# Kernel optimization log

Measured on AMD Instinct MI355X. Metric: run time of the kernel, lower is better.

The kernel has to match this reference:

```python
import jax, jax.numpy as jnp
import numpy as np

B, S, D, H = 2, 2048, 768, 12
HD = D // H
WINDOW = 64  # local_attention // 2
ROPE_THETA = 10000.0
NEG = -1e9


def setup_inputs() -> dict:
    key = jax.random.key(0)
    k1, k2, k3 = jax.random.split(key, 3)
    hidden_states = jax.random.normal(k1, (B, S, D), dtype=jnp.float32)
    Wqkv_w = jax.random.normal(k2, (3 * D, D), dtype=jnp.float32) * (D ** -0.5)
    Wo_w = jax.random.normal(k3, (D, D), dtype=jnp.float32) * (D ** -0.5)
    position_ids = jnp.broadcast_to(jnp.arange(S, dtype=jnp.int64 if jax.config.jax_enable_x64 else jnp.int32), (B, S))
    # additive sliding-window mask: 0 inside window, -1e9 outside (matches torch ModernBert mask construction)
    idx = np.arange(S)
    dist = np.abs(idx[:, None] - idx[None, :])
    sliding_window_mask = jnp.asarray(np.where(dist <= WINDOW, 0.0, NEG), dtype=jnp.float32)[None, None]  # [1,1,S,S]
    return {"hidden_states": hidden_states, "Wqkv_w": Wqkv_w, "Wo_w": Wo_w,
            "sliding_window_mask": sliding_window_mask, "position_ids": position_ids}


def _rotate_half(x):
    x1, x2 = jnp.split(x, 2, axis=-1)
    return jnp.concatenate([-x2, x1], axis=-1)


def reference(hidden_states, Wqkv_w, Wo_w, sliding_window_mask, position_ids):
    b, s, d = hidden_states.shape
    qkv = hidden_states @ Wqkv_w.T                      # [B,S,3D]
    qkv = qkv.reshape(b, s, 3, H, HD)
    q = qkv[:, :, 0].transpose(0, 2, 1, 3)              # [B,H,S,HD]
    k = qkv[:, :, 1].transpose(0, 2, 1, 3)
    v = qkv[:, :, 2].transpose(0, 2, 1, 3)
    # RoPE
    inv_freq = 1.0 / (ROPE_THETA ** (jnp.arange(0, HD, 2, dtype=jnp.float32) / HD))  # [HD/2]
    freqs = position_ids.astype(jnp.float32)[..., None] * inv_freq                   # [B,S,HD/2]
    emb = jnp.concatenate([freqs, freqs], axis=-1)                                   # [B,S,HD]
    cos = jnp.cos(emb)[:, None]                          # [B,1,S,HD]
    sin = jnp.sin(emb)[:, None]
    q = q * cos + _rotate_half(q) * sin
    k = k * cos + _rotate_half(k) * sin
    scale = HD ** -0.5
    scores = jnp.einsum('bhqd,bhkd->bhqk', q, k) * scale + sliding_window_mask       # [B,H,S,S]
    attn = jax.nn.softmax(scores.astype(jnp.float32), axis=-1).astype(q.dtype)
    out = jnp.einsum('bhqk,bhkd->bhqd', attn, v)         # [B,H,S,HD]
    out = out.transpose(0, 2, 1, 3).reshape(b, s, d)     # [B,S,D]
    return out @ Wo_w.T
```

## Files before the change

kernel.cpp:

```cpp
#include <hip/hip_runtime.h>
#include <hip/hip_bf16.h>
#include <cmath>

#define B_   2
#define S_   2048
#define D_   768
#define H_   12
#define HD_  64
#define WIN_ 64

typedef __bf16 bf16x8 __attribute__((ext_vector_type(8)));
typedef __bf16 bf16x4 __attribute__((ext_vector_type(4)));
typedef float  f32x4  __attribute__((ext_vector_type(4)));
typedef unsigned int u32;

__device__ __forceinline__ void async_ld16(const void* g, void* l) {
    __builtin_amdgcn_global_load_lds(
        (__attribute__((address_space(1))) void*)(size_t)g,
        (__attribute__((address_space(3))) void*)(u32)(size_t)l,
        16, 0, 0);
}

#define NHS (B_ * S_ * D_)
#define NWQ (3 * D_ * D_)
#define NWO (D_ * D_)

__global__ __launch_bounds__(256) void to_bf16_3(const float* __restrict__ a,
                                                 const float* __restrict__ b,
                                                 const float* __restrict__ c,
                                                 __bf16* __restrict__ oa,
                                                 __bf16* __restrict__ ob,
                                                 __bf16* __restrict__ oc) {
    const int NA = NHS / 4, NB = NWQ / 4;
    int v = blockIdx.x * 256 + threadIdx.x;
    const float* src; __bf16* dst; int idx;
    if (v < NA)           { src = a; dst = oa; idx = v; }
    else if (v < NA + NB) { src = b; dst = ob; idx = v - NA; }
    else                  { src = c; dst = oc; idx = v - NA - NB; }
    float4 x = ((const float4*)src)[idx];
    bf16x4 y = { (__bf16)x.x, (__bf16)x.y, (__bf16)x.z, (__bf16)x.w };
    *(bf16x4*)(dst + (size_t)idx * 4) = y;
}

#define GSTAGE(DA, DB, kk)                                                    \
    { const int k0_ = (kk) << 5;                                              \
      _Pragma("unroll")                                                       \
      for (int i_ = 0; i_ < 2; ++i_) {                                        \
          const int c_ = i_ * 256 + tid;                                      \
          const int row_ = c_ >> 2;                                           \
          const int cc_ = ((c_ & 3) - (row_ >> 1)) & 3;                       \
          async_ld16(A  + (size_t)(m0 + row_) * K + k0_ + cc_ * 8, (DA) + c_ * 8); \
          async_ld16(Bw + (size_t)(n0 + row_) * K + k0_ + cc_ * 8, (DB) + c_ * 8); \
      } }

#define TCOMP(SA, SB)                                                         \
    { bf16x8 af_[4], bf_[4];                                                  \
      _Pragma("unroll")                                                       \
      for (int t_ = 0; t_ < 4; ++t_) {                                        \
          af_[t_] = *(const bf16x8*)((SA) + (wr64 + t_ * 16 + fr) * 32 + sw * 8); \
          bf_[t_] = *(const bf16x8*)((SB) + (wc64 + t_ * 16 + fr) * 32 + sw * 8); \
      }                                                                       \
      _Pragma("unroll")                                                       \
      for (int ti_ = 0; ti_ < 4; ++ti_)                                       \
          _Pragma("unroll")                                                   \
          for (int tj_ = 0; tj_ < 4; ++tj_)                                   \
              acc[ti_][tj_] = __builtin_amdgcn_mfma_f32_16x16x32_bf16(        \
                  af_[ti_], bf_[tj_], acc[ti_][tj_], 0, 0, 0); }

template <int MODE>
__global__ __launch_bounds__(256) void gemm_t(const __bf16* __restrict__ A,
                                              const __bf16* __restrict__ Bw,
                                              float* __restrict__ C,
                                              __bf16* __restrict__ qkv,
                                              __bf16* __restrict__ vt,
                                              const int* __restrict__ pos,
                                              int M, int N, int K) {
    __shared__ __attribute__((aligned(16))) __bf16 sA0[4096];
    __shared__ __attribute__((aligned(16))) __bf16 sB0[4096];
    __shared__ __attribute__((aligned(16))) __bf16 sA1[4096];
    __shared__ __attribute__((aligned(16))) __bf16 sB1[4096];

    const int tid  = threadIdx.x;
    const int w    = tid >> 6;
    const int lane = tid & 63;
    const int id = blockIdx.x;
    const int m0 = (id & 31) << 7;
    const int n0 = (id >> 5) << 7;
    const int fr = lane & 15, fq = lane >> 4;
    const int sw = (fq + (fr >> 1)) & 3;
    const int wr64 = (w >> 1) * 64, wc64 = (w & 1) * 64;

    f32x4 acc[4][4] = {};

    const int nkw = K >> 5;

    GSTAGE(sA0, sB0, 0)
    __syncthreads();
    int t = 0;
    for (; t + 2 < nkw; t += 2) {
        GSTAGE(sA1, sB1, t + 1)
        TCOMP(sA0, sB0)
        __syncthreads();
        GSTAGE(sA0, sB0, t + 2)
        TCOMP(sA1, sB1)
        __syncthreads();
    }
    GSTAGE(sA1, sB1, nkw - 1)
    TCOMP(sA0, sB0)
    __syncthreads();
    TCOMP(sA1, sB1)
    __syncthreads();

    __bf16* eW = (w == 0) ? sA0 : (w == 1) ? sB0 : (w == 2) ? sA1 : sB1;
    const int mm0 = m0 + wr64, nn0 = n0 + wc64;

    if (MODE == 0) {
        float* eL = (float*)eW;
        #pragma unroll
        for (int half = 0; half < 2; ++half) {
            #pragma unroll
            for (int ti = 0; ti < 2; ++ti)
                #pragma unroll
                for (int tj = 0; tj < 4; ++tj)
                    #pragma unroll
                    for (int r = 0; r < 4; ++r)
                        eL[(ti * 16 + fq * 4 + r) * 64 + tj * 16 + fr] =
                            acc[half * 2 + ti][tj][r];
            #pragma unroll
            for (int p = 0; p < 8; ++p) {
                const int rc = p * 4 + (lane >> 4), ch = lane & 15;
                f32x4 vv = *(const f32x4*)(eL + rc * 64 + ch * 4);
                *(f32x4*)(C + (size_t)(mm0 + half * 32 + rc) * N + nn0 + ch * 4) = vv;
            }
        }
    } else if (nn0 < 2 * D_) {
        const float invf0 = __powf(10000.0f, -(float)fr * (1.0f / 32.0f));
        const float invf1 = __powf(10000.0f, -(float)(16 + fr) * (1.0f / 32.0f));
        #pragma unroll
        for (int ti = 0; ti < 4; ++ti)
            #pragma unroll
            for (int r = 0; r < 4; ++r) {
                const int row = mm0 + ti * 16 + fq * 4 + r;
                const float p = (float)pos[row];
                float s0, c0, s1, c1;
                __sincosf(p * invf0, &s0, &c0);
                __sincosf(p * invf1, &s1, &c1);
                const float x0 = acc[ti][0][r], x1 = acc[ti][2][r];
                acc[ti][0][r] = x0 * c0 - x1 * s0;
                acc[ti][2][r] = x1 * c0 + x0 * s0;
                const float y0 = acc[ti][1][r], y1 = acc[ti][3][r];
                acc[ti][1][r] = y0 * c1 - y1 * s1;
                acc[ti][3][r] = y1 * c1 + y0 * s1;
            }
        __bf16* eL = eW;
        #pragma unroll
        for (int half = 0; half < 2; ++half) {
            #pragma unroll
            for (int ti = 0; ti < 2; ++ti)
                #pragma unroll
                for (int tj = 0; tj < 4; ++tj)
                    #pragma unroll
                    for (int r = 0; r < 4; ++r)
                        eL[(ti * 16 + fq * 4 + r) * 68 + tj * 16 + fr] =
                            (__bf16)acc[half * 2 + ti][tj][r];
            #pragma unroll
            for (int p = 0; p < 4; ++p) {
                const int rq = p * 8 + (lane >> 3), ch = lane & 7;
                bf16x8 vv = *(const bf16x8*)(eL + rq * 68 + ch * 8);
                *(bf16x8*)(qkv + (size_t)(mm0 + half * 32 + rq) * (2 * D_) + nn0 + ch * 8) = vv;
            }
        }
    } else {
        const int h = (nn0 - 2 * D_) >> 6;
        const int bb = mm0 >> 11, t0 = mm0 & (S_ - 1);
        __bf16* eL = eW;
        const size_t vb = (size_t)((bb * H_ + h) * HD_) * S_ + t0;
        #pragma unroll
        for (int dh = 0; dh < 2; ++dh) {
            #pragma unroll
            for (int tj = 0; tj < 2; ++tj)
                #pragma unroll
                for (int ti = 0; ti < 4; ++ti)
                    #pragma unroll
                    for (int r = 0; r < 4; ++r)
                        eL[(tj * 16 + fr) * 68 + ti * 16 + fq * 4 + r] =
                            (__bf16)acc[ti][dh * 2 + tj][r];
            #pragma unroll
            for (int p = 0; p < 4; ++p) {
                const int d = p * 8 + (lane >> 3), ch = lane & 7;
                bf16x8 vv = *(const bf16x8*)(eL + d * 68 + ch * 8);
                *(bf16x8*)(vt + vb + (size_t)(dh * 32 + d) * S_ + ch * 8) = vv;
            }
        }
    }
}

__global__ __launch_bounds__(256) void attn_mfma(const __bf16* __restrict__ qkv,
                                                 const __bf16* __restrict__ vt,
                                                 __bf16* __restrict__ outb) {
    __shared__ __attribute__((aligned(16))) __bf16 smem[24576];
    __bf16* Ks  = smem;
    __bf16* Vts = smem + 12288;

    const int i0  = blockIdx.x * 64;
    const int h   = blockIdx.y;
    const int b   = blockIdx.z;
    const int tid = threadIdx.x;
    const int w = tid >> 6, lane = tid & 63;
    const int fr = lane & 15, fq = lane >> 4;
    const int sw = (fq + (fr >> 1)) & 3;
    const int wq0 = w * 16;

    #pragma unroll
    for (int i = 0; i < 6; ++i) {
        int c = i * 256 + tid;
        int ks = (i >= 3);
        int rem = c - ks * 768;
        int ccp = rem & 3, row = rem >> 2;
        int cc = (ccp - (row >> 1)) & 3;
        int j = i0 - 64 + row; j = min(max(j, 0), S_ - 1);
        async_ld16(qkv + ((size_t)b * S_ + j) * (2 * D_) + D_ + h * HD_ + ks * 32 + cc * 8,
                   Ks + c * 8);
    }
    const size_t vbase = (size_t)((b * H_ + h) * HD_) * S_;
    #pragma unroll
    for (int i = 0; i < 6; ++i) {
        int c = i * 256 + tid;
        int ks = c >> 8, rem = c & 255, d = rem >> 2, ccp = rem & 3;
        int cc = (ccp - (d >> 1)) & 3;
        int key = i0 - 64 + ks * 32 + cc * 8;
        key = min(max(key, 0), S_ - 8);
        async_ld16(vt + vbase + (size_t)d * S_ + key, Vts + c * 8);
    }

    const size_t qrow = ((size_t)b * S_ + i0 + wq0 + fr) * (2 * D_) + h * HD_;
    bf16x8 aq[2];
    aq[0] = *(const bf16x8*)(qkv + qrow + fq * 8);
    aq[1] = *(const bf16x8*)(qkv + qrow + 32 + fq * 8);

    __syncthreads();

    f32x4 sc[12] = {};
    #pragma unroll
    for (int nt = 0; nt < 12; ++nt) {
        #pragma unroll
        for (int ks = 0; ks < 2; ++ks) {
            bf16x8 bk = *(const bf16x8*)(Ks + (ks * 192 + nt * 16 + fr) * 32 + sw * 8);
            sc[nt] = __builtin_amdgcn_mfma_f32_16x16x32_bf16(aq[ks], bk, sc[nt], 0, 0, 0);
        }
    }

    float mx[4] = { -1e30f, -1e30f, -1e30f, -1e30f };
    #pragma unroll
    for (int nt = 0; nt < 12; ++nt) {
        const int jr = nt * 16 + fr;
        const int j  = i0 - 64 + jr;
        const bool jv = (j >= 0) && (j < S_);
        #pragma unroll
        for (int r = 0; r < 4; ++r) {
            const int ir = wq0 + fq * 4 + r + 64;
            const int dd = ir - jr;
            const bool v = jv && (dd <= WIN_) && (dd >= -WIN_);
            sc[nt][r] = v ? sc[nt][r] * 0.125f : -1e30f;
            mx[r] = fmaxf(mx[r], sc[nt][r]);
        }
    }
    #pragma unroll
    for (int r = 0; r < 4; ++r)
        #pragma unroll
        for (int off = 1; off < 16; off <<= 1)
            mx[r] = fmaxf(mx[r], __shfl_xor(mx[r], off, 64));

    float sm[4] = { 0.f, 0.f, 0.f, 0.f };
    #pragma unroll
    for (int nt = 0; nt < 12; ++nt)
        #pragma unroll
        for (int r = 0; r < 4; ++r) {
            float e = __expf(sc[nt][r] - mx[r]);
            sc[nt][r] = e;
            sm[r] += e;
        }
    #pragma unroll
    for (int r = 0; r < 4; ++r) {
        #pragma unroll
        for (int off = 1; off < 16; off <<= 1)
            sm[r] += __shfl_xor(sm[r], off, 64);
        sm[r] = 1.0f / sm[r];
    }

    __syncthreads();

    __bf16* Pw = Ks + w * 3072;
    #pragma unroll
    for (int nt = 0; nt < 12; ++nt) {
        const int ks = nt >> 1, kk = (nt & 1) * 16 + fr;
        const int kc = kk >> 3, kj = kk & 7;
        #pragma unroll
        for (int r = 0; r < 4; ++r) {
            const int pc = (kc + 2 * fq + (r >> 1)) & 3;
            Pw[(ks * 16 + fq * 4 + r) * 32 + pc * 8 + kj] = (__bf16)(sc[nt][r] * sm[r]);
        }
    }

    f32x4 oacc[4] = {};
    #pragma unroll
    for (int ks = 0; ks < 6; ++ks) {
        bf16x8 ap = *(const bf16x8*)(Pw + (ks * 16 + fr) * 32 + sw * 8);
        #pragma unroll
        for (int nt2 = 0; nt2 < 4; ++nt2) {
            bf16x8 bv = *(const bf16x8*)(Vts + (ks * 64 + nt2 * 16 + fr) * 32 + sw * 8);
            oacc[nt2] = __builtin_amdgcn_mfma_f32_16x16x32_bf16(ap, bv, oacc[nt2], 0, 0, 0);
        }
    }

    #pragma unroll
    for (int nt2 = 0; nt2 < 4; ++nt2)
        #pragma unroll
        for (int r = 0; r < 4; ++r)
            Pw[(fq * 4 + r) * 68 + nt2 * 16 + fr] = (__bf16)oacc[nt2][r];
    #pragma unroll
    for (int p = 0; p < 2; ++p) {
        const int q = p * 8 + (lane >> 3), ch = lane & 7;
        bf16x8 vv = *(const bf16x8*)(Pw + q * 68 + ch * 8);
        *(bf16x8*)(outb + ((size_t)b * S_ + i0 + wq0 + q) * D_ + h * HD_ + ch * 8) = vv;
    }
}

extern "C" void kernel_launch(void* const* d_in, const int* in_sizes, int n_in,
                              void* d_out, int out_size, void* d_ws, size_t ws_size,
                              hipStream_t stream) {
    const float* hs   = (const float*)d_in[0];
    const float* wqkv = (const float*)d_in[1];
    const float* wo   = (const float*)d_in[2];
    const int*   pos  = (const int*)d_in[4];
    float* out = (float*)d_out;

    __bf16* base    = (__bf16*)d_ws;
    __bf16* hs_bf   = base;
    __bf16* wqkv_bf = hs_bf + NHS;
    __bf16* wo_bf   = wqkv_bf + NWQ;
    __bf16* qkv     = wo_bf + NWO;
    __bf16* vt      = qkv + (size_t)(B_ * S_) * (2 * D_);
    __bf16* attn_bf = vt + (size_t)B_ * H_ * HD_ * S_;

    to_bf16_3<<<(NHS + NWQ + NWO) / 1024, 256, 0, stream>>>(
        hs, wqkv, wo, hs_bf, wqkv_bf, wo_bf);

    gemm_t<1><<<dim3(32 * (3 * D_ / 128)), 256, 0, stream>>>(
        hs_bf, wqkv_bf, nullptr, qkv, vt, pos, B_ * S_, 3 * D_, D_);

    attn_mfma<<<dim3(S_ / 64, H_, B_), 256, 0, stream>>>(qkv, vt, attn_bf);

    gemm_t<0><<<dim3(32 * (D_ / 128)), 256, 0, stream>>>(
        attn_bf, wo_bf, out, nullptr, nullptr, nullptr, B_ * S_, D_, D_);
}
```

Before: 136.3 us.

## Split GEMM K dimension across two warp groups with LDS reduction

The GEMM kernel now runs 512 threads per block, split into two 256-thread groups. Each group computes half of the K=768 reduction (12 k-steps each) in its own double-buffered LDS region, and the partial accumulators are then summed through shared memory before the epilogue. The aim is more waves per tile to hide latency, since the output GEMM launches only 192 blocks. In exchange it doubles LDS use per block, adds an extra reduction pass with two barriers, and hardcodes K=768.

```diff
diff --git a/kernel.cpp b/kernel.cpp
--- a/kernel.cpp
+++ b/kernel.cpp
@@ -42,11 +42,11 @@
     *(bf16x4*)(dst + (size_t)idx * 4) = y;
 }
 
-#define GSTAGE(DA, DB, kk)                                                    \
+#define GSTAGE2(DA, DB, kk)                                                   \
     { const int k0_ = (kk) << 5;                                              \
       _Pragma("unroll")                                                       \
       for (int i_ = 0; i_ < 2; ++i_) {                                        \
-          const int c_ = i_ * 256 + tid;                                      \
+          const int c_ = i_ * 256 + tg;                                       \
           const int row_ = c_ >> 2;                                           \
           const int cc_ = ((c_ & 3) - (row_ >> 1)) & 3;                       \
           async_ld16(A  + (size_t)(m0 + row_) * K + k0_ + cc_ * 8, (DA) + c_ * 8); \
@@ -68,50 +68,95 @@
                   af_[ti_], bf_[tj_], acc[ti_][tj_], 0, 0, 0); }
 
 template <int MODE>
-__global__ __launch_bounds__(256) void gemm_t(const __bf16* __restrict__ A,
-                                              const __bf16* __restrict__ Bw,
-                                              float* __restrict__ C,
-                                              __bf16* __restrict__ qkv,
-                                              __bf16* __restrict__ vt,
-                                              const int* __restrict__ pos,
-                                              int M, int N, int K) {
-    __shared__ __attribute__((aligned(16))) __bf16 sA0[4096];
-    __shared__ __attribute__((aligned(16))) __bf16 sB0[4096];
-    __shared__ __attribute__((aligned(16))) __bf16 sA1[4096];
-    __shared__ __attribute__((aligned(16))) __bf16 sB1[4096];
+__global__ __launch_bounds__(512) void gemm_k2(const __bf16* __restrict__ A,
+                                               const __bf16* __restrict__ Bw,
+                                               float* __restrict__ C,
+                                               __bf16* __restrict__ qkv,
+                                               __bf16* __restrict__ vt,
+                                               const int* __restrict__ pos,
+                                               int M, int N, int K) {
+    __shared__ __attribute__((aligned(16))) __bf16 sA0g0[4096];
+    __shared__ __attribute__((aligned(16))) __bf16 sB0g0[4096];
+    __shared__ __attribute__((aligned(16))) __bf16 sA1g0[4096];
+    __shared__ __attribute__((aligned(16))) __bf16 sB1g0[4096];
+    __shared__ __attribute__((aligned(16))) __bf16 sA0g1[4096];
+    __shared__ __attribute__((aligned(16))) __bf16 sB0g1[4096];
+    __shared__ __attribute__((aligned(16))) __bf16 sA1g1[4096];
+    __shared__ __attribute__((aligned(16))) __bf16 sB1g1[4096];
 
     const int tid  = threadIdx.x;
     const int w    = tid >> 6;
+    const int g    = w >> 2;
+    const int w2   = w & 3;
+    const int tg   = tid & 255;
     const int lane = tid & 63;
     const int id = blockIdx.x;
     const int m0 = (id & 31) << 7;
     const int n0 = (id >> 5) << 7;
     const int fr = lane & 15, fq = lane >> 4;
     const int sw = (fq + (fr >> 1)) & 3;
-    const int wr64 = (w >> 1) * 64, wc64 = (w & 1) * 64;
+    const int wr64 = (w2 >> 1) * 64, wc64 = (w2 & 1) * 64;
+
+    __bf16* myA0 = g ? sA0g1 : sA0g0;
+    __bf16* myB0 = g ? sB0g1 : sB0g0;
+    __bf16* myA1 = g ? sA1g1 : sA1g0;
+    __bf16* myB1 = g ? sB1g1 : sB1g0;
 
     f32x4 acc[4][4] = {};
 
-    const int nkw = K >> 5;
-
-    GSTAGE(sA0, sB0, 0)
+    const int kb = g * 12;
+
+    GSTAGE2(myA0, myB0, kb + 0)
     __syncthreads();
-    int t = 0;
-    for (; t + 2 < nkw; t += 2) {
-        GSTAGE(sA1, sB1, t + 1)
-        TCOMP(sA0, sB0)
+    for (int t = 0; t + 2 < 12; t += 2) {
+        GSTAGE2(myA1, myB1, kb + t + 1)
+        TCOMP(myA0, myB0)
         __syncthreads();
-        GSTAGE(sA0, sB0, t + 2)
-        TCOMP(sA1, sB1)
+        GSTAGE2(myA0, myB0, kb + t + 2)
+        TCOMP(myA1, myB1)
         __syncthreads();
     }
-    GSTAGE(sA1, sB1, nkw - 1)
-    TCOMP(sA0, sB0)
+    GSTAGE2(myA1, myB1, kb + 11)
+    TCOMP(myA0, myB0)
     __syncthreads();
-    TCOMP(sA1, sB1)
+    TCOMP(myA1, myB1)
     __syncthreads();
 
-    __bf16* eW = (w == 0) ? sA0 : (w == 1) ? sB0 : (w == 2) ? sA1 : sB1;
+    {
+        float* pA = (w2 == 0) ? (float*)sA0g0 : (w2 == 1) ? (float*)sA1g0
+                  : (w2 == 2) ? (float*)sA0g1 : (float*)sA1g1;
+        float* pB = (w2 == 0) ? (float*)sB0g0 : (w2 == 1) ? (float*)sB1g0
+                  : (w2 == 2) ? (float*)sB0g1 : (float*)sB1g1;
+        if (w >= 4) {
+            #pragma unroll
+            for (int ti = 0; ti < 2; ++ti)
+                #pragma unroll
+                for (int tj = 0; tj < 4; ++tj)
+                    *(f32x4*)(pA + (ti * 4 + tj) * 256 + lane * 4) = acc[ti][tj];
+            #pragma unroll
+            for (int ti = 2; ti < 4; ++ti)
+                #pragma unroll
+                for (int tj = 0; tj < 4; ++tj)
+                    *(f32x4*)(pB + ((ti - 2) * 4 + tj) * 256 + lane * 4) = acc[ti][tj];
+        }
+        __syncthreads();
+        if (w < 4) {
+            #pragma unroll
+            for (int ti = 0; ti < 2; ++ti)
+                #pragma unroll
+                for (int tj = 0; tj < 4; ++tj)
+                    acc[ti][tj] += *(const f32x4*)(pA + (ti * 4 + tj) * 256 + lane * 4);
+            #pragma unroll
+            for (int ti = 2; ti < 4; ++ti)
+                #pragma unroll
+                for (int tj = 0; tj < 4; ++tj)
+                    acc[ti][tj] += *(const f32x4*)(pB + ((ti - 2) * 4 + tj) * 256 + lane * 4);
+        }
+        __syncthreads();
+    }
+    if (w >= 4) return;
+
+    __bf16* eW = (w == 0) ? sA0g0 : (w == 1) ? sA1g0 : (w == 2) ? sA0g1 : sA1g1;
     const int mm0 = m0 + wr64, nn0 = n0 + wc64;
 
     if (MODE == 0) {
@@ -346,11 +391,11 @@
     to_bf16_3<<<(NHS + NWQ + NWO) / 1024, 256, 0, stream>>>(
         hs, wqkv, wo, hs_bf, wqkv_bf, wo_bf);
 
-    gemm_t<1><<<dim3(32 * (3 * D_ / 128)), 256, 0, stream>>>(
+    gemm_k2<1><<<dim3(32 * (3 * D_ / 128)), 512, 0, stream>>>(
         hs_bf, wqkv_bf, nullptr, qkv, vt, pos, B_ * S_, 3 * D_, D_);
 
     attn_mfma<<<dim3(S_ / 64, H_, B_), 256, 0, stream>>>(qkv, vt, attn_bf);
 
-    gemm_t<0><<<dim3(32 * (D_ / 128)), 256, 0, stream>>>(
+    gemm_k2<0><<<dim3(32 * (D_ / 128)), 512, 0, stream>>>(
         attn_bf, wo_bf, out, nullptr, nullptr, nullptr, B_ * S_, D_, D_);
 }
```

Measured after the change: 146.2 us. 1.07x slower.
